# Optimization experiments

Measured on AMD Instinct MI355X. Metric: run time of the kernel, lower is better.

The kernel has to match this reference:

```python
import jax, jax.numpy as jnp
import numpy as np

NUM_LABELS = 10  # number of distinct label values in the minibatch
EPS = 1e-8


def setup_inputs() -> dict:
    key = jax.random.key(0)
    k1, k2 = jax.random.split(key)
    z = jax.random.normal(k1, (8192, 20, 256), dtype=jnp.float32)  # [B, C, H]
    labels = jax.random.randint(k2, (8192,), 0, NUM_LABELS)  # [B]
    return {"z": z, "labels": labels}


def reference(z, labels):
    # CODI minibatch loss, positive pairs, representation space.
    # Equivalent to: for each unique label, mse(z[group] + 1e-8, mean(z[group]))
    # summed over labels. Vectorized as a single segment-mean +
    # gather-broadcast + segment-SSE pass (one traversal of z).
    z = jnp.nan_to_num(z)
    B, C, H = z.shape
    counts = jax.ops.segment_sum(
        jnp.ones((B,), dtype=z.dtype), labels, num_segments=NUM_LABELS
    )  # [K]
    sums = jax.ops.segment_sum(z, labels, num_segments=NUM_LABELS)  # [K, C, H]
    means = jnp.nan_to_num(sums / jnp.maximum(counts, 1.0)[:, None, None])
    # per-sample squared distance to its group's mean (note the +EPS as in torch)
    d = (z + EPS) - means[labels]  # [B, C, H]
    per_sample = jnp.sum(d * d, axis=(1, 2))  # [B]
    sse = jax.ops.segment_sum(per_sample, labels, num_segments=NUM_LABELS)  # [K]
    # nn.MSELoss is a mean over all elements of the group: count_k * C * H
    mse_k = sse / (jnp.maximum(counts, 1.0) * (C * H))
    # torch.unique only visits labels present in the batch -> mask empty groups
    return jnp.sum(jnp.where(counts > 0, jnp.nan_to_num(mse_k), 0.0))
```

## Files before the change

### kernel.cpp

```cpp
#include <hip/hip_runtime.h>

#define B_SZ   8192
#define CH     5120
#define CH4    1280
#define K_LAB  10
#define EPS    1e-8f
#define FLTMAX 3.402823466e38f

#define RC_N   256
#define ROWS   32
#define CC_N   4
#define CCW    320
#define NT1    320
#define NPF    4
#define NFOLD  (K_LAB * CC_N)


__device__ __forceinline__ float4 sanitize(float4 v) {
    v.x = (v.x == v.x) ? fminf(fmaxf(v.x, -FLTMAX), FLTMAX) : 0.f;
    v.y = (v.y == v.y) ? fminf(fmaxf(v.y, -FLTMAX), FLTMAX) : 0.f;
    v.z = (v.z == v.z) ? fminf(fmaxf(v.z, -FLTMAX), FLTMAX) : 0.f;
    v.w = (v.w == v.w) ? fminf(fmaxf(v.w, -FLTMAX), FLTMAX) : 0.f;
    return v;
}

__global__ __launch_bounds__(NT1) void codi_pass1(
    const float4* __restrict__ z4, const int* __restrict__ labels,
    float4* __restrict__ P_sum, float* __restrict__ P_ssq,
    int* __restrict__ P_cnt, int* __restrict__ done)
{
    const int tid  = threadIdx.x;
    const int lane = tid & 63, wid = tid >> 6;
    const int rc   = blockIdx.x >> 2;
    const int cc   = blockIdx.x & 3;

    __shared__ int   perm_s[ROWS];
    __shared__ int   starts_s[K_LAB + 1];
    __shared__ float wssq[5][K_LAB];

    if (blockIdx.x == 0 && tid == 0) *done = 0;
    if (tid < 5 * K_LAB) ((float*)wssq)[tid] = 0.f;

    if (tid < 64) {
        const int lab = (tid < ROWS) ? labels[rc * ROWS + tid] : -1;
        const unsigned long long ltm = (1ULL << lane) - 1ULL;
        int base = 0;
        #pragma unroll
        for (int k = 0; k < K_LAB; ++k) {
            unsigned long long m = __ballot(lab == k);
            int cnt = __popcll(m);
            if (tid == k) {
                starts_s[k] = base;
                if (cc == 0) P_cnt[rc * K_LAB + k] = cnt;
            }
            if (lab == k) perm_s[base + __popcll(m & ltm)] = tid;
            base += cnt;
        }
        if (tid == 0) starts_s[K_LAB] = ROWS;
    }
    __syncthreads();

    const float4* zp  = z4 + (size_t)rc * ROWS * CH4 + cc * CCW + tid;
    float4*       psb = P_sum + ((size_t)cc * RC_N + rc) * CCW + tid;

    float4 cs = make_float4(0.f, 0.f, 0.f, 0.f);
    float  cq = 0.f;
    int    kcur = 0;
    int    nb   = starts_s[1];

    #define FLUSH() do { \
        psb[(size_t)kcur * (CC_N * RC_N * CCW)] = cs; \
        float qq = cq; \
        _Pragma("unroll") \
        for (int o = 32; o > 0; o >>= 1) qq += __shfl_down(qq, o, 64); \
        if (lane == 0) wssq[wid][kcur] += qq; \
        cs = make_float4(0.f, 0.f, 0.f, 0.f); cq = 0.f; \
    } while (0)

    #define LDP(BUF, I0) do { \
        _Pragma("unroll") \
        for (int u = 0; u < NPF; ++u) \
            BUF[u] = zp[(size_t)perm_s[(I0) + u] * CH4]; \
    } while (0)

    #define CONS(BUF, I0) do { \
        _Pragma("unroll") \
        for (int u = 0; u < NPF; ++u) { \
            while ((I0) + u >= nb) {           \
                FLUSH(); ++kcur; nb = starts_s[kcur + 1]; \
            } \
            float4 t = sanitize(BUF[u]); \
            float  q = fmaf(t.x, t.x, fmaf(t.y, t.y, fmaf(t.z, t.z, t.w * t.w))); \
            cs.x += t.x; cs.y += t.y; cs.z += t.z; cs.w += t.w; cq += q; \
        } } while (0)

    float4 va[NPF], vb[NPF];
    LDP(va, 0);
    for (int i = 0; i < ROWS; i += 2 * NPF) {
        LDP(vb, i + NPF);
        CONS(va, i);
        if (i + 2 * NPF < ROWS) LDP(va, i + 2 * NPF);
        CONS(vb, i + NPF);
    }
    for (; kcur < K_LAB; ++kcur) FLUSH();
    #undef CONS
    #undef LDP
    #undef FLUSH

    __syncthreads();
    if (tid < K_LAB)
        P_ssq[(rc * CC_N + cc) * K_LAB + tid] =
            wssq[0][tid] + wssq[1][tid] + wssq[2][tid] + wssq[3][tid] + wssq[4][tid];
}

__global__ __launch_bounds__(NT1) void codi_pass2(
    const float4* __restrict__ P_sum, const float* __restrict__ P_ssq,
    const int* __restrict__ P_cnt, float* __restrict__ pn,
    float* __restrict__ ssqk, float* __restrict__ cntk,
    int* __restrict__ done, float* __restrict__ out)
{
    const int tid  = threadIdx.x;
    const int lane = tid & 63, wid = tid >> 6;
    const int fid  = blockIdx.x;
    const int fk   = fid >> 2, fcc = fid & 3;

    __shared__ float red_q[5], red_s[5];
    __shared__ int   red_n[5];
    __shared__ int   tkt;

    const float4* p = P_sum + ((size_t)(fk * CC_N + fcc) * RC_N) * CCW + tid;
    float4 s4 = make_float4(0.f, 0.f, 0.f, 0.f);
    #pragma unroll 8
    for (int rc = 0; rc < RC_N; ++rc) {
        float4 v = p[(size_t)rc * CCW];
        s4.x += v.x; s4.y += v.y; s4.z += v.z; s4.w += v.w;
    }
    float q = fmaf(s4.x, s4.x, fmaf(s4.y, s4.y, fmaf(s4.z, s4.z, s4.w * s4.w)));
    #pragma unroll
    for (int o = 32; o > 0; o >>= 1) q += __shfl_down(q, o, 64);

    float s2 = 0.f;
    int   n  = 0;
    if (fcc == 0) {
        for (int i = tid; i < RC_N * CC_N; i += NT1) s2 += P_ssq[i * K_LAB + fk];
        if (tid < RC_N) n = P_cnt[tid * K_LAB + fk];
    }
    #pragma unroll
    for (int o = 32; o > 0; o >>= 1) s2 += __shfl_down(s2, o, 64);
    #pragma unroll
    for (int o = 32; o > 0; o >>= 1) n += __shfl_down(n, o, 64);

    if (lane == 0) { red_q[wid] = q; red_s[wid] = s2; red_n[wid] = n; }
    __syncthreads();
    if (tid == 0) {
        pn[fid] = red_q[0] + red_q[1] + red_q[2] + red_q[3] + red_q[4];
        if (fcc == 0) {
            ssqk[fk] = red_s[0] + red_s[1] + red_s[2] + red_s[3] + red_s[4];
            cntk[fk] = (float)(red_n[0] + red_n[1] + red_n[2] + red_n[3] + red_n[4]);
        }
    }

    __threadfence();
    __syncthreads();
    if (tid == 0) tkt = atomicAdd(done, 1);
    __syncthreads();
    if (tkt == NFOLD - 1 && tid < 64) {
        float np4 = (tid < NFOLD) ? atomicAdd(&pn[tid], 0.f) : 0.f;
        np4 += __shfl_down(np4, 2, 64);
        np4 += __shfl_down(np4, 1, 64);
        float s2v = (tid < K_LAB) ? atomicAdd(&ssqk[tid], 0.f) : 0.f;
        float nnv = (tid < K_LAB) ? atomicAdd(&cntk[tid], 0.f) : 0.f;
        float acc = 0.f;
        for (int k = 0; k < K_LAB; ++k) {
            float np = __shfl(np4, 4 * k, 64);
            float sk = __shfl(s2v, k, 64);
            float nk = __shfl(nnv, k, 64);
            if (nk > 0.f) {
                float sse = sk - np / nk + nk * (float)CH * (EPS * EPS);
                float mse = sse / (nk * (float)CH);
                if (mse == mse) acc += mse;
            }
        }
        if (tid == 0) out[0] = acc;
    }
}

extern "C" void kernel_launch(void* const* d_in, const int* in_sizes, int n_in,
                              void* d_out, int out_size, void* d_ws, size_t ws_size,
                              hipStream_t stream) {
    const float4* z4     = (const float4*)d_in[0];
    const int*    labels = (const int*)d_in[1];

    float*  hdr   = (float*)d_ws;
    int*    done  = (int*)hdr;
    float*  pn    = hdr + 16;
    float*  ssqk  = hdr + 64;
    float*  cntk  = hdr + 80;
    int*    P_cnt = (int*)(hdr + 96);
    float*  P_ssq = hdr + 2688;
    float4* P_sum = (float4*)(hdr + 13056);

    codi_pass1<<<RC_N * CC_N, NT1, 0, stream>>>(z4, labels, P_sum, P_ssq, P_cnt, done);
    codi_pass2<<<NFOLD, NT1, 0, stream>>>(P_sum, P_ssq, P_cnt, pn, ssqk,
                                          cntk, done, (float*)d_out);
}
```

Baseline: 267.5 us.

## Process full rows per block with 640 threads instead of column-chunk blocks

```diff
diff --git a/kernel.cpp b/kernel.cpp
--- a/kernel.cpp
+++ b/kernel.cpp
@@ -9,11 +9,11 @@
 
 #define RC_N   256
 #define ROWS   32
-#define CC_N   4
-#define CCW    320
-#define NT1    320
-#define NPF    4
-#define NFOLD  (K_LAB * CC_N)
+#define NT1    640
+#define NW1    10
+#define NPF    2
+#define NT2    320
+#define NFOLD  (K_LAB * 4)
 
 
 __device__ __forceinline__ float4 sanitize(float4 v) {
@@ -31,15 +31,14 @@
 {
     const int tid  = threadIdx.x;
     const int lane = tid & 63, wid = tid >> 6;
-    const int rc   = blockIdx.x >> 2;
-    const int cc   = blockIdx.x & 3;
+    const int rc   = blockIdx.x;
 
     __shared__ int   perm_s[ROWS];
     __shared__ int   starts_s[K_LAB + 1];
-    __shared__ float wssq[5][K_LAB];
+    __shared__ float wssq[NW1][K_LAB];
 
     if (blockIdx.x == 0 && tid == 0) *done = 0;
-    if (tid < 5 * K_LAB) ((float*)wssq)[tid] = 0.f;
+    if (tid < NW1 * K_LAB) ((float*)wssq)[tid] = 0.f;
 
     if (tid < 64) {
         const int lab = (tid < ROWS) ? labels[rc * ROWS + tid] : -1;
@@ -51,7 +50,7 @@
             int cnt = __popcll(m);
             if (tid == k) {
                 starts_s[k] = base;
-                if (cc == 0) P_cnt[rc * K_LAB + k] = cnt;
+                P_cnt[rc * K_LAB + k] = cnt;
             }
             if (lab == k) perm_s[base + __popcll(m & ltm)] = tid;
             base += cnt;
@@ -60,28 +59,33 @@
     }
     __syncthreads();
 
-    const float4* zp  = z4 + (size_t)rc * ROWS * CH4 + cc * CCW + tid;
-    float4*       psb = P_sum + ((size_t)cc * RC_N + rc) * CCW + tid;
-
-    float4 cs = make_float4(0.f, 0.f, 0.f, 0.f);
-    float  cq = 0.f;
+    const float4* zp  = z4 + (size_t)rc * ROWS * CH4 + tid;
+    float4*       psb = P_sum + (size_t)rc * CH4 + tid;
+
+    float4 cs0 = make_float4(0.f, 0.f, 0.f, 0.f);
+    float4 cs1 = make_float4(0.f, 0.f, 0.f, 0.f);
+    float  cq  = 0.f;
     int    kcur = 0;
     int    nb   = starts_s[1];
 
     #define FLUSH() do { \
-        psb[(size_t)kcur * (CC_N * RC_N * CCW)] = cs; \
+        psb[(size_t)kcur * RC_N * CH4]       = cs0; \
+        psb[(size_t)kcur * RC_N * CH4 + 640] = cs1; \
         float qq = cq; \
         _Pragma("unroll") \
         for (int o = 32; o > 0; o >>= 1) qq += __shfl_down(qq, o, 64); \
         if (lane == 0) wssq[wid][kcur] += qq; \
-        cs = make_float4(0.f, 0.f, 0.f, 0.f); cq = 0.f; \
+        cs0 = make_float4(0.f, 0.f, 0.f, 0.f); \
+        cs1 = make_float4(0.f, 0.f, 0.f, 0.f); cq = 0.f; \
     } while (0)
 
     #define LDP(BUF, I0) do { \
         _Pragma("unroll") \
-        for (int u = 0; u < NPF; ++u) \
-            BUF[u] = zp[(size_t)perm_s[(I0) + u] * CH4]; \
-    } while (0)
+        for (int u = 0; u < NPF; ++u) { \
+            const size_t rb_ = (size_t)perm_s[(I0) + u] * CH4; \
+            BUF[u][0] = zp[rb_]; \
+            BUF[u][1] = zp[rb_ + 640]; \
+        } } while (0)
 
     #define CONS(BUF, I0) do { \
         _Pragma("unroll") \
@@ -89,12 +93,18 @@
             while ((I0) + u >= nb) {           \
                 FLUSH(); ++kcur; nb = starts_s[kcur + 1]; \
             } \
-            float4 t = sanitize(BUF[u]); \
-            float  q = fmaf(t.x, t.x, fmaf(t.y, t.y, fmaf(t.z, t.z, t.w * t.w))); \
-            cs.x += t.x; cs.y += t.y; cs.z += t.z; cs.w += t.w; cq += q; \
+            float4 t0 = sanitize(BUF[u][0]); \
+            float4 t1 = sanitize(BUF[u][1]); \
+            float  q  = fmaf(t0.x, t0.x, fmaf(t0.y, t0.y, \
+                        fmaf(t0.z, t0.z, t0.w * t0.w))); \
+            q = fmaf(t1.x, t1.x, fmaf(t1.y, t1.y, \
+                fmaf(t1.z, t1.z, fmaf(t1.w, t1.w, q)))); \
+            cs0.x += t0.x; cs0.y += t0.y; cs0.z += t0.z; cs0.w += t0.w; \
+            cs1.x += t1.x; cs1.y += t1.y; cs1.z += t1.z; cs1.w += t1.w; \
+            cq += q; \
         } } while (0)
 
-    float4 va[NPF], vb[NPF];
+    float4 va[NPF][2], vb[NPF][2];
     LDP(va, 0);
     for (int i = 0; i < ROWS; i += 2 * NPF) {
         LDP(vb, i + NPF);
@@ -108,12 +118,15 @@
     #undef FLUSH
 
     __syncthreads();
-    if (tid < K_LAB)
-        P_ssq[(rc * CC_N + cc) * K_LAB + tid] =
-            wssq[0][tid] + wssq[1][tid] + wssq[2][tid] + wssq[3][tid] + wssq[4][tid];
-}
-
-__global__ __launch_bounds__(NT1) void codi_pass2(
+    if (tid < K_LAB) {
+        float s = 0.f;
+        #pragma unroll
+        for (int w = 0; w < NW1; ++w) s += wssq[w][tid];
+        P_ssq[rc * K_LAB + tid] = s;
+    }
+}
+
+__global__ __launch_bounds__(NT2) void codi_pass2(
     const float4* __restrict__ P_sum, const float* __restrict__ P_ssq,
     const int* __restrict__ P_cnt, float* __restrict__ pn,
     float* __restrict__ ssqk, float* __restrict__ cntk,
@@ -122,17 +135,17 @@
     const int tid  = threadIdx.x;
     const int lane = tid & 63, wid = tid >> 6;
     const int fid  = blockIdx.x;
-    const int fk   = fid >> 2, fcc = fid & 3;
+    const int fk   = fid >> 2, fq = fid & 3;
 
     __shared__ float red_q[5], red_s[5];
     __shared__ int   red_n[5];
     __shared__ int   tkt;
 
-    const float4* p = P_sum + ((size_t)(fk * CC_N + fcc) * RC_N) * CCW + tid;
+    const float4* p = P_sum + (size_t)fk * RC_N * CH4 + fq * NT2 + tid;
     float4 s4 = make_float4(0.f, 0.f, 0.f, 0.f);
     #pragma unroll 8
     for (int rc = 0; rc < RC_N; ++rc) {
-        float4 v = p[(size_t)rc * CCW];
+        float4 v = p[(size_t)rc * CH4];
         s4.x += v.x; s4.y += v.y; s4.z += v.z; s4.w += v.w;
     }
     float q = fmaf(s4.x, s4.x, fmaf(s4.y, s4.y, fmaf(s4.z, s4.z, s4.w * s4.w)));
@@ -141,9 +154,9 @@
 
     float s2 = 0.f;
     int   n  = 0;
-    if (fcc == 0) {
-        for (int i = tid; i < RC_N * CC_N; i += NT1) s2 += P_ssq[i * K_LAB + fk];
-        if (tid < RC_N) n = P_cnt[tid * K_LAB + fk];
+    if (fq == 0 && tid < RC_N) {
+        s2 = P_ssq[tid * K_LAB + fk];
+        n  = P_cnt[tid * K_LAB + fk];
     }
     #pragma unroll
     for (int o = 32; o > 0; o >>= 1) s2 += __shfl_down(s2, o, 64);
@@ -154,7 +167,7 @@
     __syncthreads();
     if (tid == 0) {
         pn[fid] = red_q[0] + red_q[1] + red_q[2] + red_q[3] + red_q[4];
-        if (fcc == 0) {
+        if (fq == 0) {
             ssqk[fk] = red_s[0] + red_s[1] + red_s[2] + red_s[3] + red_s[4];
             cntk[fk] = (float)(red_n[0] + red_n[1] + red_n[2] + red_n[3] + red_n[4]);
         }
@@ -198,9 +211,9 @@
     float*  cntk  = hdr + 80;
     int*    P_cnt = (int*)(hdr + 96);
     float*  P_ssq = hdr + 2688;
-    float4* P_sum = (float4*)(hdr + 13056);
-
-    codi_pass1<<<RC_N * CC_N, NT1, 0, stream>>>(z4, labels, P_sum, P_ssq, P_cnt, done);
-    codi_pass2<<<NFOLD, NT1, 0, stream>>>(P_sum, P_ssq, P_cnt, pn, ssqk,
+    float4* P_sum = (float4*)(hdr + 5376);
+
+    codi_pass1<<<RC_N, NT1, 0, stream>>>(z4, labels, P_sum, P_ssq, P_cnt, done);
+    codi_pass2<<<NFOLD, NT2, 0, stream>>>(P_sum, P_ssq, P_cnt, pn, ssqk,
                                           cntk, done, (float*)d_out);
 }
```

Measured after the change: 266.6 us. About the same (-0.4%).
